# Performance work log

Measured on AMD Instinct MI355X. Metric: run time of the kernel, lower is better.

Reference implementation:

```python
import jax, jax.numpy as jnp
import numpy as np

N, E, F, H, C, B = 50000, 800000, 256, 256, 10, 64
BN_EPS = 1e-5
ATT_SLOPE = 0.2   # GATConv attention LeakyReLU
ACT_SLOPE = 0.01  # torch.nn.LeakyReLU default

def _leaky(x, slope):
    return jnp.where(x >= 0, x, slope * x)

def _gat_conv(x, src, dst, W, a_src, a_dst, b, n):
    # x:[N,Fin] -> h:[N,Fout]; single-head GATConv with self-loops already in (src,dst)
    h = x @ W
    e_src = h @ a_src  # [N]
    e_dst = h @ a_dst  # [N]
    e = _leaky(e_src[src] + e_dst[dst], ATT_SLOPE)  # [E]
    m = jax.ops.segment_max(e, dst, num_segments=n)
    ex = jnp.exp(e - m[dst])
    s = jax.ops.segment_sum(ex, dst, num_segments=n)
    alpha = ex / s[dst]
    out = jax.ops.segment_sum(alpha[:, None] * h[src], dst, num_segments=n)
    return out + b

def setup_inputs() -> dict:
    key = jax.random.key(0)
    ks = jax.random.split(key, 16)
    x = jax.random.normal(ks[0], (N, F), dtype=jnp.float32)
    edge_index = jax.random.randint(ks[1], (2, E), 0, N, dtype=jnp.int64)
    batch = jnp.sort(jax.random.randint(ks[2], (N,), 0, B, dtype=jnp.int64))
    sc = 0.05
    return {
        "x": x, "edge_index": edge_index, "batch": batch, "batch_size": B,
        "W1": jax.random.normal(ks[3], (F, H), jnp.float32) * sc,
        "a_src1": jax.random.normal(ks[4], (H,), jnp.float32) * sc,
        "a_dst1": jax.random.normal(ks[5], (H,), jnp.float32) * sc,
        "b1": jnp.zeros((H,), jnp.float32),
        "gamma": jnp.ones((H,), jnp.float32),
        "beta": jnp.zeros((H,), jnp.float32),
        "W2": jax.random.normal(ks[6], (H, H), jnp.float32) * sc,
        "a_src2": jax.random.normal(ks[7], (H,), jnp.float32) * sc,
        "a_dst2": jax.random.normal(ks[8], (H,), jnp.float32) * sc,
        "b2": jnp.zeros((H,), jnp.float32),
        "lw1": jax.random.normal(ks[9], (H, H), jnp.float32) * sc,
        "lb1": jnp.zeros((H,), jnp.float32),
        "lw2": jax.random.normal(ks[10], (H, C), jnp.float32) * sc,
        "lb2": jnp.zeros((C,), jnp.float32),
    }

def reference(x, edge_index, batch, batch_size, W1, a_src1, a_dst1, b1,
              gamma, beta, W2, a_src2, a_dst2, b2, lw1, lb1, lw2, lb2):
    n = x.shape[0]
    loops = jnp.arange(n, dtype=edge_index.dtype)
    src = jnp.concatenate([edge_index[0], loops])
    dst = jnp.concatenate([edge_index[1], loops])
    # conv1 + LeakyReLU + BatchNorm (batch statistics, biased var)
    h = _gat_conv(x, src, dst, W1, a_src1, a_dst1, b1, n)
    h = _leaky(h, ACT_SLOPE)
    mean = jnp.mean(h, axis=0)
    var = jnp.var(h, axis=0)
    h = (h - mean) * jax.lax.rsqrt(var + BN_EPS) * gamma + beta
    # conv2 + LeakyReLU
    h = _gat_conv(h, src, dst, W2, a_src2, a_dst2, b2, n)
    h = _leaky(h, ACT_SLOPE)
    # global mean pool over graphs
    sums = jax.ops.segment_sum(h, batch, num_segments=batch_size)
    cnt = jax.ops.segment_sum(jnp.ones((n,), h.dtype), batch, num_segments=batch_size)
    g = sums / jnp.maximum(cnt, 1.0)[:, None]
    # MLP head
    g = _leaky(g @ lw1 + lb1, ACT_SLOPE)
    return g @ lw2 + lb2
```

## Files before the change

kernel.cpp:

```cpp
#include <hip/hip_runtime.h>
#include <math.h>

#define N_NODES 50000
#define N_EDGES 800000
#define ETOT    (N_EDGES + N_NODES)
#define FDIM    256
#define HDIM    256
#define NGRAPH  64
#define C_OUT   10
#define BN_EPS  1e-5f
#define ATT_SLOPE 0.2f
#define ACT_SLOPE 0.01f

#define CVT_NB  ((N_NODES * HDIM / 4 + 255) / 256)
#define NBUCK   ((N_NODES + 15) / 16)
#define BCAP    512
#define SORT_NB 96
#define EPB     ((ETOT + SORT_NB - 1) / SORT_NB)

typedef __attribute__((ext_vector_type(8))) short bf16x8;
typedef __attribute__((ext_vector_type(4))) float f32x4;

__device__ __forceinline__ float leaky(float x, float s) { return x >= 0.f ? x : s * x; }

__device__ __forceinline__ float bf2f(unsigned short u) {
    return __uint_as_float((unsigned)u << 16);
}
__device__ __forceinline__ unsigned short f2bf(float f) {
    unsigned u = __float_as_uint(f);
    u += 0x7FFF + ((u >> 16) & 1);
    return (unsigned short)(u >> 16);
}
__device__ __forceinline__ float rlF(float a, int j) {
    return __uint_as_float(__builtin_amdgcn_readlane(__float_as_uint(a), j));
}

__device__ __forceinline__ void edge_sd(const int* __restrict__ ei, int e, int& s, int& d) {
    if (e < N_EDGES) { s = ei[e]; d = ei[N_EDGES + e]; }
    else             { s = e - N_EDGES; d = s; }
}

__global__ __launch_bounds__(256) void prep_k(const float* __restrict__ x,
                                              const float* __restrict__ W1,
                                              const float* __restrict__ W2,
                                              unsigned short* __restrict__ xbf,
                                              unsigned short* __restrict__ Wt1,
                                              unsigned short* __restrict__ Wt2) {
    int b = blockIdx.x;
    if (b < CVT_NB) {
        int i = b * 256 + threadIdx.x;
        if (i >= N_NODES * HDIM / 4) return;
        float4 v = *(const float4*)&x[(size_t)i * 4];
        ushort4 o;
        o.x = f2bf(v.x); o.y = f2bf(v.y); o.z = f2bf(v.z); o.w = f2bf(v.w);
        *(ushort4*)&xbf[(size_t)i * 4] = o;
    } else if (b < CVT_NB + 512) {
        int wb = b - CVT_NB;
        const float* W = (wb < 256) ? W1 : W2;
        unsigned short* Wt = (wb < 256) ? Wt1 : Wt2;
        int idx = (wb & 255) * 256 + threadIdx.x;
        int n = idx >> 8, k = idx & 255;
        Wt[idx] = f2bf(W[k * 256 + n]);
    }
}

template<bool AFFINE>
__global__ __launch_bounds__(256) void gemm_bf16(const unsigned short* __restrict__ A,
                                                 const unsigned short* __restrict__ Bt,
                                                 const float* __restrict__ scale,
                                                 const float* __restrict__ shift,
                                                 const float* __restrict__ avs,
                                                 const float* __restrict__ avd,
                                                 float* __restrict__ es,
                                                 float* __restrict__ ed,
                                                 unsigned short* __restrict__ C, int M) {
    __shared__ unsigned short Al[128 * 64];
    __shared__ unsigned short Bl[128 * 64];
    const int tid = threadIdx.x;
    const int lane = tid & 63;
    const int wid = tid >> 6;
    const int wm = wid >> 1, wn = wid & 1;
    const int row0 = blockIdx.x * 128;
    const int col0 = blockIdx.y * 128;
    const int g = lane >> 4, rl = lane & 15;
    const int srow = lane >> 3, schunk = lane & 7;

    f32x4 acc[4][4];
    #pragma unroll
    for (int m = 0; m < 4; ++m)
        #pragma unroll
        for (int n = 0; n < 4; ++n)
            acc[m][n] = (f32x4){0.f, 0.f, 0.f, 0.f};

    for (int kk = 0; kk < 256; kk += 64) {
        #pragma unroll
        for (int j = 0; j < 4; ++j) {
            int row = (wid * 4 + j) * 8 + srow;
            int sc = schunk ^ (row & 7);
            int grow = row0 + row; if (grow >= M) grow = M - 1;
            uint4 av = *(const uint4*)&A[(size_t)grow * 256 + kk + schunk * 8];
            if (AFFINE) {
                unsigned short* p = (unsigned short*)&av;
                int c0 = kk + schunk * 8;
                #pragma unroll
                for (int q = 0; q < 8; ++q)
                    p[q] = f2bf(bf2f(p[q]) * scale[c0 + q] + shift[c0 + q]);
            }
            *(uint4*)&Al[row * 64 + sc * 8] = av;
            int bcol = col0 + row;
            uint4 bv = *(const uint4*)&Bt[(size_t)bcol * 256 + kk + schunk * 8];
            *(uint4*)&Bl[row * 64 + sc * 8] = bv;
        }
        __syncthreads();
        #pragma unroll
        for (int ks = 0; ks < 2; ++ks) {
            bf16x8 af[4], bfr[4];
            int chunk = ks * 4 + g;
            #pragma unroll
            for (int m = 0; m < 4; ++m) {
                int row = wm * 64 + m * 16 + rl;
                int sc = chunk ^ (row & 7);
                af[m] = *(const bf16x8*)&Al[row * 64 + sc * 8];
            }
            #pragma unroll
            for (int n = 0; n < 4; ++n) {
                int col = wn * 64 + n * 16 + rl;
                int sc = chunk ^ (col & 7);
                bfr[n] = *(const bf16x8*)&Bl[col * 64 + sc * 8];
            }
            #pragma unroll
            for (int m = 0; m < 4; ++m)
                #pragma unroll
                for (int n = 0; n < 4; ++n)
                    acc[m][n] = __builtin_amdgcn_mfma_f32_16x16x32_bf16(af[m], bfr[n], acc[m][n], 0, 0, 0);
        }
        __syncthreads();
    }
    #pragma unroll
    for (int m = 0; m < 4; ++m) {
        #pragma unroll
        for (int n = 0; n < 4; ++n) {
            int col = col0 + wn * 64 + n * 16 + rl;
            #pragma unroll
            for (int r = 0; r < 4; ++r) {
                int row = row0 + wm * 64 + m * 16 + g * 4 + r;
                if (row < M) C[(size_t)row * 256 + col] = f2bf(acc[m][n][r]);
            }
        }
    }
    float as_[4], ad_[4];
    #pragma unroll
    for (int n = 0; n < 4; ++n) {
        int col = col0 + wn * 64 + n * 16 + rl;
        as_[n] = avs[col]; ad_[n] = avd[col];
    }
    #pragma unroll
    for (int m = 0; m < 4; ++m) {
        #pragma unroll
        for (int r = 0; r < 4; ++r) {
            float ps = 0.f, pd = 0.f;
            #pragma unroll
            for (int n = 0; n < 4; ++n) {
                float v = acc[m][n][r];
                ps += v * as_[n]; pd += v * ad_[n];
            }
            #pragma unroll
            for (int off = 1; off < 16; off <<= 1) {
                ps += __shfl_xor(ps, off);
                pd += __shfl_xor(pd, off);
            }
            if (rl == 0) {
                int row = row0 + wm * 64 + m * 16 + g * 4 + r;
                if (row < M) {
                    atomicAdd(&es[row], ps);
                    atomicAdd(&ed[row], pd);
                }
            }
        }
    }
}

__global__ __launch_bounds__(256) void count_k(const int* __restrict__ ei,
                                               int* __restrict__ hist2d) {
    __shared__ int lcnt[NBUCK];
    int t = threadIdx.x, blk = blockIdx.x;
    for (int i = t; i < NBUCK; i += 256) lcnt[i] = 0;
    __syncthreads();
    int e0 = blk * EPB, e1 = min(e0 + EPB, ETOT);
    for (int e = e0 + t; e < e1; e += 256) {
        int s, d; edge_sd(ei, e, s, d);
        atomicAdd(&lcnt[d >> 4], 1);
    }
    __syncthreads();
    int* outp = hist2d + blk * NBUCK;
    for (int i = t; i < NBUCK; i += 256) outp[i] = lcnt[i];
}

__global__ __launch_bounds__(256) void colscan_k(int* __restrict__ hist2d,
                                                 int* __restrict__ bcnt) {
    int col = blockIdx.x * 256 + threadIdx.x;
    if (col >= NBUCK) return;
    int run = 0;
    for (int b = 0; b < SORT_NB; ++b) {
        int idx = b * NBUCK + col;
        int c = hist2d[idx];
        hist2d[idx] = run;
        run += c;
    }
    bcnt[col] = run;
}

__global__ __launch_bounds__(256) void scan_buckets(const int* __restrict__ bcnt,
                                                    int* __restrict__ bbase,
                                                    int* __restrict__ row_ptr) {
    __shared__ int s[256];
    constexpr int PER = (NBUCK + 255) / 256;
    int t = threadIdx.x;
    int loc[PER];
    int sum = 0;
    #pragma unroll
    for (int i = 0; i < PER; ++i) {
        int idx = t * PER + i;
        loc[i] = sum;
        sum += (idx < NBUCK) ? bcnt[idx] : 0;
    }
    s[t] = sum;
    __syncthreads();
    #pragma unroll
    for (int off = 1; off < 256; off <<= 1) {
        int add = (t >= off) ? s[t - off] : 0;
        __syncthreads();
        s[t] += add;
        __syncthreads();
    }
    int base = (t > 0) ? s[t - 1] : 0;
    #pragma unroll
    for (int i = 0; i < PER; ++i) {
        int idx = t * PER + i;
        if (idx < NBUCK) bbase[idx] = base + loc[i];
    }
    if (t == 0) row_ptr[N_NODES] = ETOT;
}

__global__ __launch_bounds__(256) void scatter2_k(const int* __restrict__ ei,
                                                  const int* __restrict__ hist2d,
                                                  int* __restrict__ bstore) {
    __shared__ int lcur[NBUCK];
    __shared__ int lbase[NBUCK];
    int t = threadIdx.x, blk = blockIdx.x;
    const int* boff = hist2d + blk * NBUCK;
    for (int i = t; i < NBUCK; i += 256) { lcur[i] = 0; lbase[i] = boff[i]; }
    __syncthreads();
    int e0 = blk * EPB, e1 = min(e0 + EPB, ETOT);
    for (int e = e0 + t; e < e1; e += 256) {
        int s, d; edge_sd(ei, e, s, d);
        int b = d >> 4;
        int r = atomicAdd(&lcur[b], 1);
        int pos = lbase[b] + r;
        if (pos < BCAP) bstore[(size_t)b * BCAP + pos] = s | ((d & 15) << 16);
    }
}

__global__ __launch_bounds__(256) void place_k(const int* __restrict__ bcnt,
                                               const int* __restrict__ bbase,
                                               const int* __restrict__ bstore,
                                               int* __restrict__ row_ptr,
                                               int* __restrict__ csr_src) {
    __shared__ int h16[16], e16[16], c16[16];
    int b = blockIdx.x, t = threadIdx.x;
    if (t < 16) { h16[t] = 0; c16[t] = 0; }
    __syncthreads();
    int sz = bcnt[b]; if (sz > BCAP) sz = BCAP;
    int base = bbase[b];
    const int* bs = bstore + (size_t)b * BCAP;
    int v0 = -1, v1 = -1;
    if (t < sz)       { v0 = bs[t];       atomicAdd(&h16[v0 >> 16], 1); }
    if (t + 256 < sz) { v1 = bs[t + 256]; atomicAdd(&h16[v1 >> 16], 1); }
    __syncthreads();
    if (t == 0) {
        int run = 0;
        #pragma unroll
        for (int j = 0; j < 16; ++j) { e16[j] = run; run += h16[j]; }
    }
    __syncthreads();
    if (t < 16) {
        int d = b * 16 + t;
        if (d < N_NODES) row_ptr[d] = base + e16[t];
    }
    if (v0 >= 0) {
        int dl = v0 >> 16;
        int pos = base + e16[dl] + atomicAdd(&c16[dl], 1);
        csr_src[pos] = v0 & 0xFFFF;
    }
    if (v1 >= 0) {
        int dl = v1 >> 16;
        int pos = base + e16[dl] + atomicAdd(&c16[dl], 1);
        csr_src[pos] = v1 & 0xFFFF;
    }
}

__device__ __forceinline__ void gather4(const unsigned short* __restrict__ hl,
                                        float a, int src, int lim,
                                        float4& A0, float4& A1, float4& A2, float4& A3) {
    int j = 0;
    for (; j + 3 < lim; j += 4) {
        float w0 = rlF(a, j + 0), w1 = rlF(a, j + 1), w2 = rlF(a, j + 2), w3 = rlF(a, j + 3);
        int s0 = __builtin_amdgcn_readlane(src, j + 0);
        int s1 = __builtin_amdgcn_readlane(src, j + 1);
        int s2 = __builtin_amdgcn_readlane(src, j + 2);
        int s3 = __builtin_amdgcn_readlane(src, j + 3);
        ushort4 v0 = *(const ushort4*)&hl[(size_t)s0 * HDIM];
        ushort4 v1 = *(const ushort4*)&hl[(size_t)s1 * HDIM];
        ushort4 v2 = *(const ushort4*)&hl[(size_t)s2 * HDIM];
        ushort4 v3 = *(const ushort4*)&hl[(size_t)s3 * HDIM];
        A0.x += w0 * bf2f(v0.x); A0.y += w0 * bf2f(v0.y); A0.z += w0 * bf2f(v0.z); A0.w += w0 * bf2f(v0.w);
        A1.x += w1 * bf2f(v1.x); A1.y += w1 * bf2f(v1.y); A1.z += w1 * bf2f(v1.z); A1.w += w1 * bf2f(v1.w);
        A2.x += w2 * bf2f(v2.x); A2.y += w2 * bf2f(v2.y); A2.z += w2 * bf2f(v2.z); A2.w += w2 * bf2f(v2.w);
        A3.x += w3 * bf2f(v3.x); A3.y += w3 * bf2f(v3.y); A3.z += w3 * bf2f(v3.z); A3.w += w3 * bf2f(v3.w);
    }
    for (; j < lim; ++j) {
        float w = rlF(a, j);
        int s = __builtin_amdgcn_readlane(src, j);
        ushort4 v = *(const ushort4*)&hl[(size_t)s * HDIM];
        A0.x += w * bf2f(v.x); A0.y += w * bf2f(v.y); A0.z += w * bf2f(v.z); A0.w += w * bf2f(v.w);
    }
}

__global__ __launch_bounds__(256) void dst_agg(const int* __restrict__ row_ptr,
                                               const int* __restrict__ csr_src,
                                               const float* __restrict__ es,
                                               const float* __restrict__ ed,
                                               const unsigned short* __restrict__ h,
                                               const float* __restrict__ bias,
                                               unsigned short* __restrict__ outb) {
    int d = blockIdx.x * 4 + (threadIdx.x >> 6);
    int lane = threadIdx.x & 63;
    if (d >= N_NODES) return;
    float4 b4 = *(const float4*)&bias[lane * 4];
    int start = row_ptr[d], end = row_ptr[d + 1];
    int deg = end - start;
    float edv = ed[d];
    const unsigned short* hl = h + lane * 4;
    float4 A0 = {0,0,0,0}, A1 = {0,0,0,0}, A2 = {0,0,0,0}, A3 = {0,0,0,0};
    float ssum = 0.f;

    if (deg > 0 && deg <= 64) {
        int src = 0; float v = -INFINITY;
        if (lane < deg) {
            src = csr_src[start + lane];
            v = leaky(es[src] + edv, ATT_SLOPE);
        }
        float m = v;
        #pragma unroll
        for (int off = 32; off; off >>= 1) m = fmaxf(m, __shfl_xor(m, off));
        float a = (lane < deg) ? expf(v - m) : 0.f;
        ssum = a;
        gather4(hl, a, src, deg, A0, A1, A2, A3);
    } else if (deg > 64) {
        float m = -INFINITY;
        for (int base = start; base < end; base += 64) {
            int idx = base + lane;
            if (idx < end) m = fmaxf(m, leaky(es[csr_src[idx]] + edv, ATT_SLOPE));
        }
        #pragma unroll
        for (int off = 32; off; off >>= 1) m = fmaxf(m, __shfl_xor(m, off));
        for (int base = start; base < end; base += 64) {
            int idx = base + lane;
            int src = 0; float a = 0.f;
            if (idx < end) {
                src = csr_src[idx];
                a = expf(leaky(es[src] + edv, ATT_SLOPE) - m);
            }
            ssum += a;
            int lim = end - base; if (lim > 64) lim = 64;
            gather4(hl, a, src, lim, A0, A1, A2, A3);
        }
    } else {
        ssum = 1.f;
    }
    #pragma unroll
    for (int off = 32; off; off >>= 1) ssum += __shfl_xor(ssum, off);
    float inv = (deg > 0) ? (1.f / ssum) : 0.f;
    float4 acc;
    acc.x = (A0.x + A1.x) + (A2.x + A3.x);
    acc.y = (A0.y + A1.y) + (A2.y + A3.y);
    acc.z = (A0.z + A1.z) + (A2.z + A3.z);
    acc.w = (A0.w + A1.w) + (A2.w + A3.w);
    ushort4 o;
    o.x = f2bf(leaky(acc.x * inv + b4.x, ACT_SLOPE));
    o.y = f2bf(leaky(acc.y * inv + b4.y, ACT_SLOPE));
    o.z = f2bf(leaky(acc.z * inv + b4.z, ACT_SLOPE));
    o.w = f2bf(leaky(acc.w * inv + b4.w, ACT_SLOPE));
    *(ushort4*)&outb[(size_t)d * HDIM + lane * 4] = o;
}

__global__ __launch_bounds__(256) void bn_stats_k(const unsigned short* __restrict__ buf,
                                                  float* __restrict__ csum,
                                                  float* __restrict__ csq) {
    int t = threadIdx.x;
    int rows_per = (N_NODES + gridDim.x - 1) / gridDim.x;
    int r0 = blockIdx.x * rows_per;
    int r1 = min(r0 + rows_per, N_NODES);
    float sum = 0.f, sq = 0.f;
    for (int r = r0; r < r1; ++r) {
        float v = bf2f(buf[(size_t)r * HDIM + t]);
        sum += v; sq += v * v;
    }
    atomicAdd(&csum[t], sum);
    atomicAdd(&csq[t], sq);
}

__global__ __launch_bounds__(256) void bn_param(const float* __restrict__ csum,
                                                const float* __restrict__ csq,
                                                const float* __restrict__ gamma,
                                                const float* __restrict__ beta,
                                                float* __restrict__ scale,
                                                float* __restrict__ shift) {
    int t = threadIdx.x;
    float mean = csum[t] / (float)N_NODES;
    float var = csq[t] / (float)N_NODES - mean * mean;
    float sc = gamma[t] * rsqrtf(var + BN_EPS);
    scale[t] = sc;
    shift[t] = beta[t] - mean * sc;
}

__global__ __launch_bounds__(256) void post_pool(const unsigned short* __restrict__ buf,
                                                 const int* __restrict__ batch,
                                                 float* __restrict__ gsum,
                                                 float* __restrict__ gcnt) {
    int t = threadIdx.x;
    int rows_per = (N_NODES + gridDim.x - 1) / gridDim.x;
    int r0 = blockIdx.x * rows_per;
    int r1 = min(r0 + rows_per, N_NODES);
    if (r0 >= r1) return;
    int curb = -1; float acc = 0.f; int cnt = 0;
    for (int r = r0; r < r1; ++r) {
        int bb = batch[r];
        if (bb != curb) {
            if (curb >= 0) {
                atomicAdd(&gsum[(size_t)curb * HDIM + t], acc);
                if (t == 0) atomicAdd(&gcnt[curb], (float)cnt);
            }
            curb = bb; acc = 0.f; cnt = 0;
        }
        acc += bf2f(buf[(size_t)r * HDIM + t]);
        cnt++;
    }
    if (curb >= 0) {
        atomicAdd(&gsum[(size_t)curb * HDIM + t], acc);
        if (t == 0) atomicAdd(&gcnt[curb], (float)cnt);
    }
}

__global__ __launch_bounds__(256) void mlp_head(const float* __restrict__ gsum,
                                                const float* __restrict__ gcnt,
                                                const float* __restrict__ lw1,
                                                const float* __restrict__ lb1,
                                                const float* __restrict__ lw2,
                                                const float* __restrict__ lb2,
                                                float* __restrict__ out) {
    __shared__ float g[HDIM];
    __shared__ float hid[HDIM];
    int b = blockIdx.x, t = threadIdx.x;
    float cnt = fmaxf(gcnt[b], 1.f);
    g[t] = gsum[(size_t)b * HDIM + t] / cnt;
    __syncthreads();
    float acc = lb1[t];
    for (int k = 0; k < HDIM; ++k) acc += g[k] * lw1[(size_t)k * HDIM + t];
    hid[t] = leaky(acc, ACT_SLOPE);
    __syncthreads();
    if (t < C_OUT) {
        float o = lb2[t];
        for (int k = 0; k < HDIM; ++k) o += hid[k] * lw2[(size_t)k * C_OUT + t];
        out[(size_t)b * C_OUT + t] = o;
    }
}

extern "C" void kernel_launch(void* const* d_in, const int* in_sizes, int n_in,
                              void* d_out, int out_size, void* d_ws, size_t ws_size,
                              hipStream_t stream) {
    const float* x      = (const float*)d_in[0];
    const int*   ei     = (const int*)d_in[1];
    const int*   batch  = (const int*)d_in[2];
    const float* W1     = (const float*)d_in[4];
    const float* a_src1 = (const float*)d_in[5];
    const float* a_dst1 = (const float*)d_in[6];
    const float* b1     = (const float*)d_in[7];
    const float* gamma  = (const float*)d_in[8];
    const float* beta   = (const float*)d_in[9];
    const float* W2     = (const float*)d_in[10];
    const float* a_src2 = (const float*)d_in[11];
    const float* a_dst2 = (const float*)d_in[12];
    const float* b2     = (const float*)d_in[13];
    const float* lw1    = (const float*)d_in[14];
    const float* lb1    = (const float*)d_in[15];
    const float* lw2    = (const float*)d_in[16];
    const float* lb2    = (const float*)d_in[17];
    float* out = (float*)d_out;

    const size_t NH = (size_t)N_NODES * HDIM;
    char* ws = (char*)d_ws;
    unsigned short* xbf     = (unsigned short*)ws; ws += NH * 2;
    unsigned short* hbf     = (unsigned short*)ws; ws += NH * 2;
    unsigned short* aggbf   = (unsigned short*)ws; ws += NH * 2;
    unsigned short* Wt1     = (unsigned short*)ws; ws += 65536 * 2;
    unsigned short* Wt2     = (unsigned short*)ws; ws += 65536 * 2;
    float* e_src   = (float*)ws; ws += N_NODES * 4;
    float* e_dst   = (float*)ws; ws += N_NODES * 4;
    float* csum    = (float*)ws; ws += HDIM * 4;
    float* csq     = (float*)ws; ws += HDIM * 4;
    float* scale   = (float*)ws; ws += HDIM * 4;
    float* shift   = (float*)ws; ws += HDIM * 4;
    float* gsum    = (float*)ws; ws += NGRAPH * HDIM * 4;
    float* gcnt    = (float*)ws; ws += NGRAPH * 4;
    int*   row_ptr = (int*)ws;   ws += (N_NODES + 1) * 4;
    int*   bcnt    = (int*)ws;   ws += NBUCK * 4;
    int*   bbase   = (int*)ws;   ws += NBUCK * 4;
    int*   hist2d  = (int*)ws;   ws += (size_t)SORT_NB * NBUCK * 4;
    int*   csr_src = (int*)ws;   ws += (size_t)ETOT * 4;
    int*   bstore  = (int*)ws;   ws += (size_t)NBUCK * BCAP * 4;

    const int wave4_blocks = (N_NODES + 3) / 4;
    dim3 ggrid((N_NODES + 127) / 128, 2);

    count_k<<<SORT_NB, 256, 0, stream>>>(ei, hist2d);
    colscan_k<<<(NBUCK + 255) / 256, 256, 0, stream>>>(hist2d, bcnt);
    scan_buckets<<<1, 256, 0, stream>>>(bcnt, bbase, row_ptr);
    scatter2_k<<<SORT_NB, 256, 0, stream>>>(ei, hist2d, bstore);
    place_k<<<NBUCK, 256, 0, stream>>>(bcnt, bbase, bstore, row_ptr, csr_src);

    prep_k<<<CVT_NB + 512, 256, 0, stream>>>(x, W1, W2, xbf, Wt1, Wt2);

    hipMemsetAsync(e_src, 0, (size_t)N_NODES * 8, stream);
    gemm_bf16<false><<<ggrid, 256, 0, stream>>>(xbf, Wt1, nullptr, nullptr,
                                                a_src1, a_dst1, e_src, e_dst, hbf, N_NODES);
    dst_agg<<<wave4_blocks, 256, 0, stream>>>(row_ptr, csr_src, e_src, e_dst, hbf, b1, aggbf);

    hipMemsetAsync(csum, 0, HDIM * 8, stream);
    bn_stats_k<<<256, 256, 0, stream>>>(aggbf, csum, csq);
    bn_param<<<1, 256, 0, stream>>>(csum, csq, gamma, beta, scale, shift);

    hipMemsetAsync(e_src, 0, (size_t)N_NODES * 8, stream);
    gemm_bf16<true><<<ggrid, 256, 0, stream>>>(aggbf, Wt2, scale, shift,
                                               a_src2, a_dst2, e_src, e_dst, hbf, N_NODES);
    dst_agg<<<wave4_blocks, 256, 0, stream>>>(row_ptr, csr_src, e_src, e_dst, hbf, b2, aggbf);

    hipMemsetAsync(gsum, 0, (size_t)(NGRAPH * HDIM + NGRAPH) * 4, stream);
    post_pool<<<256, 256, 0, stream>>>(aggbf, batch, gsum, gcnt);

    mlp_head<<<NGRAPH, 256, 0, stream>>>(gsum, gcnt, lw1, lb1, lw2, lb2, out);
}
```

Baseline: 366.4 us.

## Fuse fp32-to-bf16 conversion into GEMM, replace score atomics, widen gather loads

The first GEMM now reads fp32 x directly and converts it to bf16 while staging into LDS, which removes the separate conversion pass and the xbf buffer. Attention score partials are reduced in LDS and written non-atomically into four per-column-block arrays, so the memsets and global atomics go away. The edge gather in dst_agg now splits the wave into two halves that each load 16-byte rows for alternating edges and combine with a cross-half shuffle. In exchange the GEMM reads twice as many A bytes, and dst_agg performs extra loads to sum the score partials.

```diff
diff --git a/kernel.cpp b/kernel.cpp
--- a/kernel.cpp
+++ b/kernel.cpp
@@ -12,7 +12,6 @@
 #define ATT_SLOPE 0.2f
 #define ACT_SLOPE 0.01f
 
-#define CVT_NB  ((N_NODES * HDIM / 4 + 255) / 256)
 #define NBUCK   ((N_NODES + 15) / 16)
 #define BCAP    512
 #define SORT_NB 96
@@ -40,42 +39,30 @@
     else             { s = e - N_EDGES; d = s; }
 }
 
-__global__ __launch_bounds__(256) void prep_k(const float* __restrict__ x,
-                                              const float* __restrict__ W1,
+__global__ __launch_bounds__(256) void prep_w(const float* __restrict__ W1,
                                               const float* __restrict__ W2,
-                                              unsigned short* __restrict__ xbf,
                                               unsigned short* __restrict__ Wt1,
                                               unsigned short* __restrict__ Wt2) {
-    int b = blockIdx.x;
-    if (b < CVT_NB) {
-        int i = b * 256 + threadIdx.x;
-        if (i >= N_NODES * HDIM / 4) return;
-        float4 v = *(const float4*)&x[(size_t)i * 4];
-        ushort4 o;
-        o.x = f2bf(v.x); o.y = f2bf(v.y); o.z = f2bf(v.z); o.w = f2bf(v.w);
-        *(ushort4*)&xbf[(size_t)i * 4] = o;
-    } else if (b < CVT_NB + 512) {
-        int wb = b - CVT_NB;
-        const float* W = (wb < 256) ? W1 : W2;
-        unsigned short* Wt = (wb < 256) ? Wt1 : Wt2;
-        int idx = (wb & 255) * 256 + threadIdx.x;
-        int n = idx >> 8, k = idx & 255;
-        Wt[idx] = f2bf(W[k * 256 + n]);
-    }
-}
-
-template<bool AFFINE>
-__global__ __launch_bounds__(256) void gemm_bf16(const unsigned short* __restrict__ A,
+    int wb = blockIdx.x;
+    const float* W = (wb < 256) ? W1 : W2;
+    unsigned short* Wt = (wb < 256) ? Wt1 : Wt2;
+    int idx = (wb & 255) * 256 + threadIdx.x;
+    int n = idx >> 8, k = idx & 255;
+    Wt[idx] = f2bf(W[k * 256 + n]);
+}
+
+template<bool AFFINE, bool FROMF32>
+__global__ __launch_bounds__(256) void gemm_bf16(const void* __restrict__ Avp,
                                                  const unsigned short* __restrict__ Bt,
                                                  const float* __restrict__ scale,
                                                  const float* __restrict__ shift,
                                                  const float* __restrict__ avs,
                                                  const float* __restrict__ avd,
-                                                 float* __restrict__ es,
-                                                 float* __restrict__ ed,
+                                                 float* __restrict__ e_part,
                                                  unsigned short* __restrict__ C, int M) {
     __shared__ unsigned short Al[128 * 64];
     __shared__ unsigned short Bl[128 * 64];
+    __shared__ float lred[2][128][2];
     const int tid = threadIdx.x;
     const int lane = tid & 63;
     const int wid = tid >> 6;
@@ -98,13 +85,24 @@
             int row = (wid * 4 + j) * 8 + srow;
             int sc = schunk ^ (row & 7);
             int grow = row0 + row; if (grow >= M) grow = M - 1;
-            uint4 av = *(const uint4*)&A[(size_t)grow * 256 + kk + schunk * 8];
-            if (AFFINE) {
+            uint4 av;
+            if (FROMF32) {
+                const float* Af = (const float*)Avp;
+                float4 f0 = *(const float4*)&Af[(size_t)grow * 256 + kk + schunk * 8];
+                float4 f1 = *(const float4*)&Af[(size_t)grow * 256 + kk + schunk * 8 + 4];
                 unsigned short* p = (unsigned short*)&av;
-                int c0 = kk + schunk * 8;
-                #pragma unroll
-                for (int q = 0; q < 8; ++q)
-                    p[q] = f2bf(bf2f(p[q]) * scale[c0 + q] + shift[c0 + q]);
+                p[0] = f2bf(f0.x); p[1] = f2bf(f0.y); p[2] = f2bf(f0.z); p[3] = f2bf(f0.w);
+                p[4] = f2bf(f1.x); p[5] = f2bf(f1.y); p[6] = f2bf(f1.z); p[7] = f2bf(f1.w);
+            } else {
+                const unsigned short* Ab = (const unsigned short*)Avp;
+                av = *(const uint4*)&Ab[(size_t)grow * 256 + kk + schunk * 8];
+                if (AFFINE) {
+                    unsigned short* p = (unsigned short*)&av;
+                    int c0 = kk + schunk * 8;
+                    #pragma unroll
+                    for (int q = 0; q < 8; ++q)
+                        p[q] = f2bf(bf2f(p[q]) * scale[c0 + q] + shift[c0 + q]);
+                }
             }
             *(uint4*)&Al[row * 64 + sc * 8] = av;
             int bcol = col0 + row;
@@ -170,12 +168,20 @@
                 pd += __shfl_xor(pd, off);
             }
             if (rl == 0) {
-                int row = row0 + wm * 64 + m * 16 + g * 4 + r;
-                if (row < M) {
-                    atomicAdd(&es[row], ps);
-                    atomicAdd(&ed[row], pd);
-                }
-            }
+                int lr = wm * 64 + m * 16 + g * 4 + r;
+                lred[wn][lr][0] = ps;
+                lred[wn][lr][1] = pd;
+            }
+        }
+    }
+    __syncthreads();
+    if (tid < 128) {
+        int row = row0 + tid;
+        if (row < M) {
+            e_part[(size_t)blockIdx.y * N_NODES + row] =
+                lred[0][tid][0] + lred[1][tid][0];
+            e_part[(size_t)(2 + blockIdx.y) * N_NODES + row] =
+                lred[0][tid][1] + lred[1][tid][1];
         }
     }
 }
@@ -299,68 +305,66 @@
     }
 }
 
-__device__ __forceinline__ void gather4(const unsigned short* __restrict__ hl,
-                                        float a, int src, int lim,
-                                        float4& A0, float4& A1, float4& A2, float4& A3) {
-    int j = 0;
-    for (; j + 3 < lim; j += 4) {
-        float w0 = rlF(a, j + 0), w1 = rlF(a, j + 1), w2 = rlF(a, j + 2), w3 = rlF(a, j + 3);
-        int s0 = __builtin_amdgcn_readlane(src, j + 0);
-        int s1 = __builtin_amdgcn_readlane(src, j + 1);
-        int s2 = __builtin_amdgcn_readlane(src, j + 2);
-        int s3 = __builtin_amdgcn_readlane(src, j + 3);
-        ushort4 v0 = *(const ushort4*)&hl[(size_t)s0 * HDIM];
-        ushort4 v1 = *(const ushort4*)&hl[(size_t)s1 * HDIM];
-        ushort4 v2 = *(const ushort4*)&hl[(size_t)s2 * HDIM];
-        ushort4 v3 = *(const ushort4*)&hl[(size_t)s3 * HDIM];
-        A0.x += w0 * bf2f(v0.x); A0.y += w0 * bf2f(v0.y); A0.z += w0 * bf2f(v0.z); A0.w += w0 * bf2f(v0.w);
-        A1.x += w1 * bf2f(v1.x); A1.y += w1 * bf2f(v1.y); A1.z += w1 * bf2f(v1.z); A1.w += w1 * bf2f(v1.w);
-        A2.x += w2 * bf2f(v2.x); A2.y += w2 * bf2f(v2.y); A2.z += w2 * bf2f(v2.z); A2.w += w2 * bf2f(v2.w);
-        A3.x += w3 * bf2f(v3.x); A3.y += w3 * bf2f(v3.y); A3.z += w3 * bf2f(v3.z); A3.w += w3 * bf2f(v3.w);
-    }
-    for (; j < lim; ++j) {
-        float w = rlF(a, j);
-        int s = __builtin_amdgcn_readlane(src, j);
-        ushort4 v = *(const ushort4*)&hl[(size_t)s * HDIM];
-        A0.x += w * bf2f(v.x); A0.y += w * bf2f(v.y); A0.z += w * bf2f(v.z); A0.w += w * bf2f(v.w);
-    }
+__device__ __forceinline__ void pair_acc(const unsigned short* __restrict__ h,
+                                         int hl, int half, float a, int src, int j0,
+                                         float* accv) {
+    float wA = rlF(a, j0);
+    float wB = rlF(a, j0 + 1);
+    int sA = __builtin_amdgcn_readlane(src, j0);
+    int sB = __builtin_amdgcn_readlane(src, j0 + 1);
+    float w = half ? wB : wA;
+    int   s = half ? sB : sA;
+    uint4 hv = *(const uint4*)&h[(size_t)s * HDIM + hl * 8];
+    const unsigned short* p = (const unsigned short*)&hv;
+    #pragma unroll
+    for (int k = 0; k < 8; ++k) accv[k] += w * bf2f(p[k]);
 }
 
 __global__ __launch_bounds__(256) void dst_agg(const int* __restrict__ row_ptr,
                                                const int* __restrict__ csr_src,
-                                               const float* __restrict__ es,
-                                               const float* __restrict__ ed,
+                                               const float* __restrict__ e_part,
                                                const unsigned short* __restrict__ h,
                                                const float* __restrict__ bias,
                                                unsigned short* __restrict__ outb) {
     int d = blockIdx.x * 4 + (threadIdx.x >> 6);
     int lane = threadIdx.x & 63;
     if (d >= N_NODES) return;
-    float4 b4 = *(const float4*)&bias[lane * 4];
+    const float* es0 = e_part;
+    const float* es1 = e_part + N_NODES;
+    const float* ed0 = e_part + 2 * N_NODES;
+    const float* ed1 = e_part + 3 * N_NODES;
+    int half = lane >> 5, hl = lane & 31;
     int start = row_ptr[d], end = row_ptr[d + 1];
     int deg = end - start;
-    float edv = ed[d];
-    const unsigned short* hl = h + lane * 4;
-    float4 A0 = {0,0,0,0}, A1 = {0,0,0,0}, A2 = {0,0,0,0}, A3 = {0,0,0,0};
+    float edv = ed0[d] + ed1[d];
+    float accv[8] = {0.f, 0.f, 0.f, 0.f, 0.f, 0.f, 0.f, 0.f};
     float ssum = 0.f;
 
     if (deg > 0 && deg <= 64) {
         int src = 0; float v = -INFINITY;
         if (lane < deg) {
             src = csr_src[start + lane];
-            v = leaky(es[src] + edv, ATT_SLOPE);
+            v = leaky(es0[src] + es1[src] + edv, ATT_SLOPE);
         }
         float m = v;
         #pragma unroll
         for (int off = 32; off; off >>= 1) m = fmaxf(m, __shfl_xor(m, off));
         float a = (lane < deg) ? expf(v - m) : 0.f;
         ssum = a;
-        gather4(hl, a, src, deg, A0, A1, A2, A3);
+        int j = 0;
+        for (; j + 2 < deg; j += 4) {
+            pair_acc(h, hl, half, a, src, j, accv);
+            pair_acc(h, hl, half, a, src, j + 2, accv);
+        }
+        if (j < deg) pair_acc(h, hl, half, a, src, j, accv);
     } else if (deg > 64) {
         float m = -INFINITY;
         for (int base = start; base < end; base += 64) {
             int idx = base + lane;
-            if (idx < end) m = fmaxf(m, leaky(es[csr_src[idx]] + edv, ATT_SLOPE));
+            if (idx < end) {
+                int s = csr_src[idx];
+                m = fmaxf(m, leaky(es0[s] + es1[s] + edv, ATT_SLOPE));
+            }
         }
         #pragma unroll
         for (int off = 32; off; off >>= 1) m = fmaxf(m, __shfl_xor(m, off));
@@ -369,11 +373,16 @@
             int src = 0; float a = 0.f;
             if (idx < end) {
                 src = csr_src[idx];
-                a = expf(leaky(es[src] + edv, ATT_SLOPE) - m);
+                a = expf(leaky(es0[src] + es1[src] + edv, ATT_SLOPE) - m);
             }
             ssum += a;
             int lim = end - base; if (lim > 64) lim = 64;
-            gather4(hl, a, src, lim, A0, A1, A2, A3);
+            int j = 0;
+            for (; j + 2 < lim; j += 4) {
+                pair_acc(h, hl, half, a, src, j, accv);
+                pair_acc(h, hl, half, a, src, j + 2, accv);
+            }
+            if (j < lim) pair_acc(h, hl, half, a, src, j, accv);
         }
     } else {
         ssum = 1.f;
@@ -381,17 +390,18 @@
     #pragma unroll
     for (int off = 32; off; off >>= 1) ssum += __shfl_xor(ssum, off);
     float inv = (deg > 0) ? (1.f / ssum) : 0.f;
-    float4 acc;
-    acc.x = (A0.x + A1.x) + (A2.x + A3.x);
-    acc.y = (A0.y + A1.y) + (A2.y + A3.y);
-    acc.z = (A0.z + A1.z) + (A2.z + A3.z);
-    acc.w = (A0.w + A1.w) + (A2.w + A3.w);
-    ushort4 o;
-    o.x = f2bf(leaky(acc.x * inv + b4.x, ACT_SLOPE));
-    o.y = f2bf(leaky(acc.y * inv + b4.y, ACT_SLOPE));
-    o.z = f2bf(leaky(acc.z * inv + b4.z, ACT_SLOPE));
-    o.w = f2bf(leaky(acc.w * inv + b4.w, ACT_SLOPE));
-    *(ushort4*)&outb[(size_t)d * HDIM + lane * 4] = o;
+    #pragma unroll
+    for (int k = 0; k < 8; ++k) accv[k] += __shfl_xor(accv[k], 32);
+    if (half == 0) {
+        float4 bA = *(const float4*)&bias[hl * 8];
+        float4 bB = *(const float4*)&bias[hl * 8 + 4];
+        float bb[8] = {bA.x, bA.y, bA.z, bA.w, bB.x, bB.y, bB.z, bB.w};
+        unsigned short o[8];
+        #pragma unroll
+        for (int k = 0; k < 8; ++k)
+            o[k] = f2bf(leaky(accv[k] * inv + bb[k], ACT_SLOPE));
+        *(uint4*)&outb[(size_t)d * HDIM + hl * 8] = *(uint4*)o;
+    }
 }
 
 __global__ __launch_bounds__(256) void bn_stats_k(const unsigned short* __restrict__ buf,
@@ -500,13 +510,11 @@
 
     const size_t NH = (size_t)N_NODES * HDIM;
     char* ws = (char*)d_ws;
-    unsigned short* xbf     = (unsigned short*)ws; ws += NH * 2;
     unsigned short* hbf     = (unsigned short*)ws; ws += NH * 2;
     unsigned short* aggbf   = (unsigned short*)ws; ws += NH * 2;
     unsigned short* Wt1     = (unsigned short*)ws; ws += 65536 * 2;
     unsigned short* Wt2     = (unsigned short*)ws; ws += 65536 * 2;
-    float* e_src   = (float*)ws; ws += N_NODES * 4;
-    float* e_dst   = (float*)ws; ws += N_NODES * 4;
+    float* e_part  = (float*)ws; ws += (size_t)4 * N_NODES * 4;
     float* csum    = (float*)ws; ws += HDIM * 4;
     float* csq     = (float*)ws; ws += HDIM * 4;
     float* scale   = (float*)ws; ws += HDIM * 4;
@@ -529,21 +537,19 @@
     scatter2_k<<<SORT_NB, 256, 0, stream>>>(ei, hist2d, bstore);
     place_k<<<NBUCK, 256, 0, stream>>>(bcnt, bbase, bstore, row_ptr, csr_src);
 
-    prep_k<<<CVT_NB + 512, 256, 0, stream>>>(x, W1, W2, xbf, Wt1, Wt2);
-
-    hipMemsetAsync(e_src, 0, (size_t)N_NODES * 8, stream);
-    gemm_bf16<false><<<ggrid, 256, 0, stream>>>(xbf, Wt1, nullptr, nullptr,
-                                                a_src1, a_dst1, e_src, e_dst, hbf, N_NODES);
-    dst_agg<<<wave4_blocks, 256, 0, stream>>>(row_ptr, csr_src, e_src, e_dst, hbf, b1, aggbf);
+    prep_w<<<512, 256, 0, stream>>>(W1, W2, Wt1, Wt2);
+
+    gemm_bf16<false, true><<<ggrid, 256, 0, stream>>>(x, Wt1, nullptr, nullptr,
+                                                      a_src1, a_dst1, e_part, hbf, N_NODES);
+    dst_agg<<<wave4_blocks, 256, 0, stream>>>(row_ptr, csr_src, e_part, hbf, b1, aggbf);
 
     hipMemsetAsync(csum, 0, HDIM * 8, stream);
     bn_stats_k<<<256, 256, 0, stream>>>(aggbf, csum, csq);
     bn_param<<<1, 256, 0, stream>>>(csum, csq, gamma, beta, scale, shift);
 
-    hipMemsetAsync(e_src, 0, (size_t)N_NODES * 8, stream);
-    gemm_bf16<true><<<ggrid, 256, 0, stream>>>(aggbf, Wt2, scale, shift,
-                                               a_src2, a_dst2, e_src, e_dst, hbf, N_NODES);
-    dst_agg<<<wave4_blocks, 256, 0, stream>>>(row_ptr, csr_src, e_src, e_dst, hbf, b2, aggbf);
+    gemm_bf16<true, false><<<ggrid, 256, 0, stream>>>(aggbf, Wt2, scale, shift,
+                                                      a_src2, a_dst2, e_part, hbf, N_NODES);
+    dst_agg<<<wave4_blocks, 256, 0, stream>>>(row_ptr, csr_src, e_part, hbf, b2, aggbf);
 
     hipMemsetAsync(gsum, 0, (size_t)(NGRAPH * HDIM + NGRAPH) * 4, stream);
     post_pool<<<256, 256, 0, stream>>>(aggbf, batch, gsum, gcnt);
```

New measurement: 366.9 us. Within noise of the previous version (+0.1%).

## Fuse x bf16 conversion into GEMM, use full-width 128x256 tiles, drop atomics

Applied to the files above, without the earlier changes.

The separate x-to-bf16 conversion pass is removed, and the first GEMM reads fp32 x directly and converts it while staging into LDS. The GEMM now uses 512-thread blocks covering all 256 output columns. Each A tile is therefore loaded once rather than twice, and the attention dot products can be reduced in LDS and written directly. This removes the two memsets and the global atomics on e_src/e_dst. The cost is more LDS per block, which may lower occupancy, plus double-width fp32 loads for A in layer one.

```diff
diff --git a/kernel.cpp b/kernel.cpp
--- a/kernel.cpp
+++ b/kernel.cpp
@@ -12,7 +12,6 @@
 #define ATT_SLOPE 0.2f
 #define ACT_SLOPE 0.01f
 
-#define CVT_NB  ((N_NODES * HDIM / 4 + 255) / 256)
 #define NBUCK   ((N_NODES + 15) / 16)
 #define BCAP    512
 #define SORT_NB 96
@@ -40,32 +39,20 @@
     else             { s = e - N_EDGES; d = s; }
 }
 
-__global__ __launch_bounds__(256) void prep_k(const float* __restrict__ x,
-                                              const float* __restrict__ W1,
+__global__ __launch_bounds__(256) void prep_w(const float* __restrict__ W1,
                                               const float* __restrict__ W2,
-                                              unsigned short* __restrict__ xbf,
                                               unsigned short* __restrict__ Wt1,
                                               unsigned short* __restrict__ Wt2) {
-    int b = blockIdx.x;
-    if (b < CVT_NB) {
-        int i = b * 256 + threadIdx.x;
-        if (i >= N_NODES * HDIM / 4) return;
-        float4 v = *(const float4*)&x[(size_t)i * 4];
-        ushort4 o;
-        o.x = f2bf(v.x); o.y = f2bf(v.y); o.z = f2bf(v.z); o.w = f2bf(v.w);
-        *(ushort4*)&xbf[(size_t)i * 4] = o;
-    } else if (b < CVT_NB + 512) {
-        int wb = b - CVT_NB;
-        const float* W = (wb < 256) ? W1 : W2;
-        unsigned short* Wt = (wb < 256) ? Wt1 : Wt2;
-        int idx = (wb & 255) * 256 + threadIdx.x;
-        int n = idx >> 8, k = idx & 255;
-        Wt[idx] = f2bf(W[k * 256 + n]);
-    }
-}
-
-template<bool AFFINE>
-__global__ __launch_bounds__(256) void gemm_bf16(const unsigned short* __restrict__ A,
+    int wb = blockIdx.x;
+    const float* W = (wb < 256) ? W1 : W2;
+    unsigned short* Wt = (wb < 256) ? Wt1 : Wt2;
+    int idx = (wb & 255) * 256 + threadIdx.x;
+    int n = idx >> 8, k = idx & 255;
+    Wt[idx] = f2bf(W[k * 256 + n]);
+}
+
+template<bool AFFINE, bool FROMF32>
+__global__ __launch_bounds__(512) void gemm_bf16(const void* __restrict__ Avp,
                                                  const unsigned short* __restrict__ Bt,
                                                  const float* __restrict__ scale,
                                                  const float* __restrict__ shift,
@@ -75,15 +62,14 @@
                                                  float* __restrict__ ed,
                                                  unsigned short* __restrict__ C, int M) {
     __shared__ unsigned short Al[128 * 64];
-    __shared__ unsigned short Bl[128 * 64];
+    __shared__ unsigned short Bl[256 * 64];
+    __shared__ float lred[4][128][2];
     const int tid = threadIdx.x;
     const int lane = tid & 63;
     const int wid = tid >> 6;
-    const int wm = wid >> 1, wn = wid & 1;
+    const int wm = wid >> 2, wn = wid & 3;
     const int row0 = blockIdx.x * 128;
-    const int col0 = blockIdx.y * 128;
     const int g = lane >> 4, rl = lane & 15;
-    const int srow = lane >> 3, schunk = lane & 7;
 
     f32x4 acc[4][4];
     #pragma unroll
@@ -94,22 +80,39 @@
 
     for (int kk = 0; kk < 256; kk += 64) {
         #pragma unroll
+        for (int j = 0; j < 2; ++j) {
+            int idx = j * 512 + tid;
+            int row = idx >> 3, chunk = idx & 7;
+            int sc = chunk ^ (row & 7);
+            int grow = row0 + row; if (grow >= M) grow = M - 1;
+            uint4 av;
+            if (FROMF32) {
+                const float* Af = (const float*)Avp;
+                float4 f0 = *(const float4*)&Af[(size_t)grow * 256 + kk + chunk * 8];
+                float4 f1 = *(const float4*)&Af[(size_t)grow * 256 + kk + chunk * 8 + 4];
+                unsigned short* p = (unsigned short*)&av;
+                p[0] = f2bf(f0.x); p[1] = f2bf(f0.y); p[2] = f2bf(f0.z); p[3] = f2bf(f0.w);
+                p[4] = f2bf(f1.x); p[5] = f2bf(f1.y); p[6] = f2bf(f1.z); p[7] = f2bf(f1.w);
+            } else {
+                const unsigned short* Ab = (const unsigned short*)Avp;
+                av = *(const uint4*)&Ab[(size_t)grow * 256 + kk + chunk * 8];
+                if (AFFINE) {
+                    unsigned short* p = (unsigned short*)&av;
+                    int c0 = kk + chunk * 8;
+                    #pragma unroll
+                    for (int q = 0; q < 8; ++q)
+                        p[q] = f2bf(bf2f(p[q]) * scale[c0 + q] + shift[c0 + q]);
+                }
+            }
+            *(uint4*)&Al[row * 64 + sc * 8] = av;
+        }
+        #pragma unroll
         for (int j = 0; j < 4; ++j) {
-            int row = (wid * 4 + j) * 8 + srow;
-            int sc = schunk ^ (row & 7);
-            int grow = row0 + row; if (grow >= M) grow = M - 1;
-            uint4 av = *(const uint4*)&A[(size_t)grow * 256 + kk + schunk * 8];
-            if (AFFINE) {
-                unsigned short* p = (unsigned short*)&av;
-                int c0 = kk + schunk * 8;
-                #pragma unroll
-                for (int q = 0; q < 8; ++q)
-                    p[q] = f2bf(bf2f(p[q]) * scale[c0 + q] + shift[c0 + q]);
-            }
-            *(uint4*)&Al[row * 64 + sc * 8] = av;
-            int bcol = col0 + row;
-            uint4 bv = *(const uint4*)&Bt[(size_t)bcol * 256 + kk + schunk * 8];
-            *(uint4*)&Bl[row * 64 + sc * 8] = bv;
+            int idx = j * 512 + tid;
+            int col = idx >> 3, chunk = idx & 7;
+            int sc = chunk ^ (col & 7);
+            uint4 bv = *(const uint4*)&Bt[(size_t)col * 256 + kk + chunk * 8];
+            *(uint4*)&Bl[col * 64 + sc * 8] = bv;
         }
         __syncthreads();
         #pragma unroll
@@ -140,7 +143,7 @@
     for (int m = 0; m < 4; ++m) {
         #pragma unroll
         for (int n = 0; n < 4; ++n) {
-            int col = col0 + wn * 64 + n * 16 + rl;
+            int col = wn * 64 + n * 16 + rl;
             #pragma unroll
             for (int r = 0; r < 4; ++r) {
                 int row = row0 + wm * 64 + m * 16 + g * 4 + r;
@@ -151,7 +154,7 @@
     float as_[4], ad_[4];
     #pragma unroll
     for (int n = 0; n < 4; ++n) {
-        int col = col0 + wn * 64 + n * 16 + rl;
+        int col = wn * 64 + n * 16 + rl;
         as_[n] = avs[col]; ad_[n] = avd[col];
     }
     #pragma unroll
@@ -170,12 +173,18 @@
                 pd += __shfl_xor(pd, off);
             }
             if (rl == 0) {
-                int row = row0 + wm * 64 + m * 16 + g * 4 + r;
-                if (row < M) {
-                    atomicAdd(&es[row], ps);
-                    atomicAdd(&ed[row], pd);
-                }
-            }
+                int lr = wm * 64 + m * 16 + g * 4 + r;
+                lred[wn][lr][0] = ps;
+                lred[wn][lr][1] = pd;
+            }
+        }
+    }
+    __syncthreads();
+    if (tid < 128) {
+        int row = row0 + tid;
+        if (row < M) {
+            es[row] = (lred[0][tid][0] + lred[1][tid][0]) + (lred[2][tid][0] + lred[3][tid][0]);
+            ed[row] = (lred[0][tid][1] + lred[1][tid][1]) + (lred[2][tid][1] + lred[3][tid][1]);
         }
     }
 }
@@ -500,13 +509,12 @@
 
     const size_t NH = (size_t)N_NODES * HDIM;
     char* ws = (char*)d_ws;
-    unsigned short* xbf     = (unsigned short*)ws; ws += NH * 2;
     unsigned short* hbf     = (unsigned short*)ws; ws += NH * 2;
     unsigned short* aggbf   = (unsigned short*)ws; ws += NH * 2;
     unsigned short* Wt1     = (unsigned short*)ws; ws += 65536 * 2;
     unsigned short* Wt2     = (unsigned short*)ws; ws += 65536 * 2;
-    float* e_src   = (float*)ws; ws += N_NODES * 4;
-    float* e_dst   = (float*)ws; ws += N_NODES * 4;
+    float* es      = (float*)ws; ws += N_NODES * 4;
+    float* ed      = (float*)ws; ws += N_NODES * 4;
     float* csum    = (float*)ws; ws += HDIM * 4;
     float* csq     = (float*)ws; ws += HDIM * 4;
     float* scale   = (float*)ws; ws += HDIM * 4;
@@ -521,7 +529,7 @@
     int*   bstore  = (int*)ws;   ws += (size_t)NBUCK * BCAP * 4;
 
     const int wave4_blocks = (N_NODES + 3) / 4;
-    dim3 ggrid((N_NODES + 127) / 128, 2);
+    const int gemm_blocks = (N_NODES + 127) / 128;
 
     count_k<<<SORT_NB, 256, 0, stream>>>(ei, hist2d);
     colscan_k<<<(NBUCK + 255) / 256, 256, 0, stream>>>(hist2d, bcnt);
@@ -529,21 +537,19 @@
     scatter2_k<<<SORT_NB, 256, 0, stream>>>(ei, hist2d, bstore);
     place_k<<<NBUCK, 256, 0, stream>>>(bcnt, bbase, bstore, row_ptr, csr_src);
 
-    prep_k<<<CVT_NB + 512, 256, 0, stream>>>(x, W1, W2, xbf, Wt1, Wt2);
-
-    hipMemsetAsync(e_src, 0, (size_t)N_NODES * 8, stream);
-    gemm_bf16<false><<<ggrid, 256, 0, stream>>>(xbf, Wt1, nullptr, nullptr,
-                                                a_src1, a_dst1, e_src, e_dst, hbf, N_NODES);
-    dst_agg<<<wave4_blocks, 256, 0, stream>>>(row_ptr, csr_src, e_src, e_dst, hbf, b1, aggbf);
+    prep_w<<<512, 256, 0, stream>>>(W1, W2, Wt1, Wt2);
+
+    gemm_bf16<false, true><<<gemm_blocks, 512, 0, stream>>>(x, Wt1, nullptr, nullptr,
+                                                            a_src1, a_dst1, es, ed, hbf, N_NODES);
+    dst_agg<<<wave4_blocks, 256, 0, stream>>>(row_ptr, csr_src, es, ed, hbf, b1, aggbf);
 
     hipMemsetAsync(csum, 0, HDIM * 8, stream);
     bn_stats_k<<<256, 256, 0, stream>>>(aggbf, csum, csq);
     bn_param<<<1, 256, 0, stream>>>(csum, csq, gamma, beta, scale, shift);
 
-    hipMemsetAsync(e_src, 0, (size_t)N_NODES * 8, stream);
-    gemm_bf16<true><<<ggrid, 256, 0, stream>>>(aggbf, Wt2, scale, shift,
-                                               a_src2, a_dst2, e_src, e_dst, hbf, N_NODES);
-    dst_agg<<<wave4_blocks, 256, 0, stream>>>(row_ptr, csr_src, e_src, e_dst, hbf, b2, aggbf);
+    gemm_bf16<true, false><<<gemm_blocks, 512, 0, stream>>>(aggbf, Wt2, scale, shift,
+                                                            a_src2, a_dst2, es, ed, hbf, N_NODES);
+    dst_agg<<<wave4_blocks, 256, 0, stream>>>(row_ptr, csr_src, es, ed, hbf, b2, aggbf);
 
     hipMemsetAsync(gsum, 0, (size_t)(NGRAPH * HDIM + NGRAPH) * 4, stream);
     post_pool<<<256, 256, 0, stream>>>(aggbf, batch, gsum, gcnt);
```

Result: faster. 342.0 us (-6.7%).
